# Performance work log

Hardware: AMD Instinct MI355X
Metric: run time of the kernel (lower is better)

The kernel has to match this reference:

```python
import jax, jax.numpy as jnp
import numpy as np
from jax import lax

INF = 1e4          # 'infinite' distance for chamfer transform
THETA0 = 3.0       # boundary weight decay
K_CHAMFER = 24     # exp(-24/3)~3e-4: distances beyond this are negligible
SQ2 = 1.4142135


def setup_inputs() -> dict:
    key = jax.random.key(0)
    k1, k2 = jax.random.split(key)
    inputs = jax.random.normal(k1, (32, 1, 512, 512), jnp.float32)
    targets = (jax.random.uniform(k2, (32, 1, 512, 512)) < 0.3).astype(jnp.float32)
    alpha = jnp.float32(0.25)   # config.FOCAL_ALPHA, learnable
    gamma = jnp.float32(3.0)    # config.FOCAL_GAMMA, learnable
    return {"inputs": inputs, "targets": targets, "alpha": alpha, "gamma": gamma}


def _boundary_weight(t):
    """t: (B,H,W) binary mask -> boundary-distance weight exp(-d/theta0)+0.1.
    Faithful GPU-friendly replacement for cv2 findContours/drawContours(th=3)
    + distanceTransform(L2, 3): morphological external gradient, dilated once
    (3px band), then truncated chamfer distance transform."""
    B, H, W = t.shape
    tp = jnp.pad(t, ((0, 0), (1, 1), (1, 1)))  # pad 0 so border object pixels count as edge
    eroded = lax.reduce_window(tp, jnp.inf, lax.min, (1, 3, 3), (1, 1, 1), 'VALID')
    edge = t * (1.0 - eroded)                  # contour pixels (thickness 1)
    ep = jnp.pad(edge, ((0, 0), (1, 1), (1, 1)))
    bmask = lax.reduce_window(ep, -jnp.inf, lax.max, (1, 3, 3), (1, 1, 1), 'VALID')  # thickness 3

    d = jnp.where(bmask > 0.5, 0.0, INF)
    offs = [(-1, -1, SQ2), (-1, 0, 1.0), (-1, 1, SQ2), (0, -1, 1.0),
            (0, 1, 1.0), (1, -1, SQ2), (1, 0, 1.0), (1, 1, SQ2)]

    def shift(x, di, dj):
        xp = jnp.pad(x, ((0, 0), (max(di, 0), max(-di, 0)), (max(dj, 0), max(-dj, 0))),
                     constant_values=INF)
        return xp[:, max(-di, 0):max(-di, 0) + H, max(-dj, 0):max(-dj, 0) + W]

    def step(dc, _):
        nd = dc
        for di, dj, c in offs:
            nd = jnp.minimum(nd, shift(dc, di, dj) + c)
        return nd, None

    d, _ = lax.scan(step, d, None, length=K_CHAMFER)
    return jnp.exp(-jnp.minimum(d, INF) / THETA0) + 0.1


def reference(inputs, targets, alpha, gamma):
    probs = jax.nn.sigmoid(inputs)
    smooth = 1e-6
    eps = 1e-7

    # --- dice (smp binary, from_logits, global dims=(0,2)) ---
    inter = jnp.sum(probs * targets)
    card = jnp.sum(probs) + jnp.sum(targets)
    dice_score = (2.0 * inter + smooth) / jnp.maximum(card + smooth, eps)
    dice = jnp.where(jnp.sum(targets) > 0, 1.0 - dice_score, 0.0)

    # --- adaptive focal ---
    a = jnp.clip(alpha, 0.1, 0.9)
    g = jnp.clip(gamma, 1.0, 5.0)
    st = targets * 0.95 + 0.025  # label smoothing
    bce_el = st * jax.nn.softplus(-inputs) + (1.0 - st) * jax.nn.softplus(inputs)
    p_t = st * probs + (1.0 - st) * (1.0 - probs)
    a_t = st * a + (1.0 - st) * (1.0 - a)
    focal = jnp.mean(a_t * (1.0 - p_t) ** g * bce_el)

    # --- BCEWithLogits, pos_weight=7 ---
    bce = jnp.mean(7.0 * targets * jax.nn.softplus(-inputs)
                   + (1.0 - targets) * jax.nn.softplus(inputs))

    # --- dynamic tversky, class_weight=3 ---
    pos_ratio = jnp.mean(targets)
    da = 0.7 * (1.0 + pos_ratio)
    db = 0.3 * (2.0 - pos_ratio)
    tp = inter
    fn = jnp.sum(targets * (1.0 - probs))
    fp = jnp.sum((1.0 - targets) * probs) * 3.0
    tversky = 1.0 - (tp + smooth) / (tp + da * fn + db * fp + smooth)

    # --- boundary loss (preds detached in original) ---
    t2 = targets[:, 0]
    w = _boundary_weight(t2)
    p = jnp.clip(lax.stop_gradient(probs[:, 0]), 1e-7, 1.0 - 1e-7)
    bnd_bce = -(t2 * jnp.log(p) + (1.0 - t2) * jnp.log1p(-p))
    boundary = jnp.mean(jnp.mean(bnd_bce * w, axis=(1, 2)))

    return 0.35 * dice + 0.25 * focal + 0.15 * bce + 0.15 * tversky + 0.1 * boundary
```

## Files before the change

kernel.cpp:

```cpp
#include <hip/hip_runtime.h>

typedef unsigned long long u64;
typedef unsigned int u32;

#define HH 512
#define WW 512
#define BATCH 32
#define NPIX (BATCH*HH*WW)
#define NQ (NPIX/4)
#define NWORDS (NPIX/64)
#define WPI (HH*WW/64)
#define WPR (WW/64)
#define MAIN_BLOCKS 4096
#define MAIN_THREADS 256
#define MAIN_IT 2
#define QCAP 1024
#define WINMASK ((((1ULL<<49)-1)) << 8)

__device__ __forceinline__ float hw_exp2(float x) { return __builtin_amdgcn_exp2f(x); }
__device__ __forceinline__ float hw_log2(float x) { return __builtin_amdgcn_logf(x); }

__global__ __launch_bounds__(256) void pack_kernel(const float* __restrict__ t,
                                                   u64* __restrict__ bits) {
    int stride = gridDim.x * 256;
    for (int i = blockIdx.x * 256 + threadIdx.x; i < NPIX; i += stride) {
        u64 m = __ballot(t[i] > 0.5f);
        if ((threadIdx.x & 63) == 0) bits[i >> 6] = m;
    }
}

__global__ __launch_bounds__(256) void stencil_kernel(const u64* __restrict__ tb,
                                                      u64* __restrict__ bmbits) {
    int wi = blockIdx.x * 256 + threadIdx.x;
    if (wi >= NWORDS) return;
    int img = wi >> 12;
    int loc = wi & (WPI - 1);
    int y = loc >> 3;
    int wx = loc & (WPR - 1);
    const u64* base = tb + img * WPI;

    u64 w[5][5];
    #pragma unroll
    for (int r = 0; r < 5; ++r) {
        int yy = y + r - 2;
        #pragma unroll
        for (int c = 0; c < 5; ++c) {
            int xx = wx + c - 2;
            w[r][c] = (yy >= 0 && yy < HH && xx >= 0 && xx < WPR) ? base[yy * WPR + xx] : 0ULL;
        }
    }

    u64 ha[5][3];
    #pragma unroll
    for (int r = 0; r < 5; ++r)
        #pragma unroll
        for (int j = 0; j < 3; ++j) {
            u64 C = w[r][j + 1], L = w[r][j], R = w[r][j + 2];
            ha[r][j] = ((C << 1) | (L >> 63)) & C & ((C >> 1) | (R << 63));
        }

    u64 eg[3][3];
    #pragma unroll
    for (int i = 0; i < 3; ++i)
        #pragma unroll
        for (int j = 0; j < 3; ++j) {
            u64 er = ha[i][j] & ha[i + 1][j] & ha[i + 2][j];
            eg[i][j] = w[i + 1][j + 1] & ~er;
        }

    u64 out = 0ULL;
    #pragma unroll
    for (int i = 0; i < 3; ++i) {
        u64 E = eg[i][1], L = eg[i][0], R = eg[i][2];
        out |= ((E << 1) | (L >> 63)) | E | ((E >> 1) | (R << 63));
    }
    bmbits[wi] = out;
}

__device__ __forceinline__ int rowscan(const u64* __restrict__ row, int x0) {
    int s = x0 - 32;
    int wi = s >> 6;
    int sh = s & 63;
    u64 lo = (wi >= 0 && wi < WPR) ? row[wi] : 0ULL;
    u64 hi = ((wi + 1) < WPR) ? row[wi + 1] : 0ULL;
    u64 win = sh ? ((lo >> sh) | (hi << (64 - sh))) : lo;
    win &= WINMASK;
    u64 left = win << 32;
    u64 right = win >> 32;
    int dl = left ? (__builtin_clzll(left) + 1) : 99;
    int dr = right ? __builtin_ctzll(right) : 99;
    return dl < dr ? dl : dr;
}

__device__ __forceinline__ float search_weight(const u64* __restrict__ img, int pix) {
    const float L2E = 1.44269504f;
    int x0 = pix & (WW - 1);
    int y0 = (pix >> 9) & (HH - 1);
    float best = 1e9f;
    for (int ady = 0; ady <= 24; ++ady) {
        if ((float)ady >= best) break;
        int hd = 99;
        int yU = y0 - ady;
        if (yU >= 0) hd = rowscan(img + yU * WPR, x0);
        int yD = y0 + ady;
        if (ady > 0 && yD < HH) {
            int h2 = rowscan(img + yD * WPR, x0);
            hd = h2 < hd ? h2 : hd;
        }
        if (hd <= 24) {
            float h = (float)hd, ay = (float)ady;
            float mx = fmaxf(h, ay), mn = fminf(h, ay);
            best = fminf(best, mx + 0.4142135f * mn);
        }
    }
    return (best < 1e8f) ? (hw_exp2(best * (-L2E / 3.0f)) + 0.1f) : 0.1f;
}

__global__ __launch_bounds__(MAIN_THREADS, 6) void main_kernel(
        const float4* __restrict__ x4, const u64* __restrict__ tbits,
        const u64* __restrict__ bmbits,
        const float* __restrict__ alpha_p, const float* __restrict__ gamma_p,
        double* __restrict__ partials) {
    __shared__ u64 qdata[QCAP];
    __shared__ int lcount;
    __shared__ double red[4][6];

    if (threadIdx.x == 0) lcount = 0;
    __syncthreads();

    const float a = fminf(fmaxf(alpha_p[0], 0.1f), 0.9f);
    const float one_m_a = 1.0f - a;
    const float g = fminf(fmaxf(gamma_p[0], 1.0f), 5.0f);
    const float gr = rintf(g);
    const bool gint = (g == gr);
    const int gi = (int)gr;
    const float LOGCLIP = 16.11809565f;
    const float L2E = 1.44269504f;
    const float LN2 = 0.69314718f;

    float s_p = 0.f, s_pt = 0.f, s_f = 0.f, s_b = 0.f, s_bnd_bm = 0.f, s_bnd_q = 0.f;
    int c_t = 0;

    #pragma unroll 1
    for (int it = 0; it < MAIN_IT; ++it) {
        int q = (it * MAIN_BLOCKS + blockIdx.x) * MAIN_THREADS + threadIdx.x;
        float4 xv4 = x4[q];
        int pix0 = q * 4;
        int sh = pix0 & 63;
        u64 tw = tbits[pix0 >> 6] >> sh;
        u64 bw = bmbits[pix0 >> 6] >> sh;
        float xs[4] = {xv4.x, xv4.y, xv4.z, xv4.w};

        #pragma unroll
        for (int k = 0; k < 4; ++k) {
            float xv = xs[k];
            int tb = (int)((tw >> k) & 1ULL);
            int bm = (int)((bw >> k) & 1ULL);

            float ax = fabsf(xv);
            float e  = hw_exp2(ax * -L2E);
            float rc = __builtin_amdgcn_rcpf(1.0f + e);
            float p  = (xv >= 0.0f) ? rc : e * rc;
            float l1pe = hw_log2(1.0f + e) * LN2;
            float sp_neg = fmaxf(-xv, 0.0f) + l1pe;
            float sp_pos = sp_neg + xv;

            float bce_el = sp_neg + (tb ? 0.025f : 0.975f) * xv;
            float q95 = 0.95f * p;
            float u   = tb ? (0.975f - q95) : (0.025f + q95);
            float a_t = tb ? a : one_m_a;
            float pw;
            if (gint) {
                float u2 = u * u;
                pw = (gi == 1) ? u : (gi == 2) ? u2 : (gi == 3) ? u2 * u
                   : (gi == 4) ? u2 * u2 : u2 * u2 * u;
            } else {
                pw = hw_exp2(g * hw_log2(u));
            }
            float focal_el = a_t * pw * bce_el;

            float bce2 = tb ? 7.0f * sp_neg : sp_pos;
            float bnd  = fminf(tb ? sp_neg : sp_pos, LOGCLIP);

            if (bm) {
                s_bnd_bm += bnd;
            } else {
                int slot = atomicAdd(&lcount, 1);
                if (slot < QCAP) {
                    qdata[slot] = ((u64)(u32)(pix0 + k) << 32) | (u64)__float_as_uint(bnd);
                } else {
                    s_bnd_q += bnd * search_weight(bmbits + ((pix0 + k) >> 18) * WPI, pix0 + k);
                }
            }

            s_p  += p;
            c_t  += tb;
            s_pt += tb ? p : 0.0f;
            s_f  += focal_el;
            s_b  += bce2;
        }
    }

    __syncthreads();
    int n = lcount < QCAP ? lcount : QCAP;
    for (int j = threadIdx.x; j < n; j += MAIN_THREADS) {
        u64 v = qdata[j];
        int pix = (int)(v >> 32);
        float bnd = __uint_as_float((u32)v);
        s_bnd_q += bnd * search_weight(bmbits + (pix >> 18) * WPI, pix);
    }

    double d_p = s_p, d_t = (double)c_t, d_pt = s_pt, d_f = s_f, d_b = s_b;
    double d_bnd = (double)s_bnd_bm * 1.1 + (double)s_bnd_q;

    #pragma unroll
    for (int off = 32; off > 0; off >>= 1) {
        d_p   += __shfl_down(d_p, off);
        d_t   += __shfl_down(d_t, off);
        d_pt  += __shfl_down(d_pt, off);
        d_f   += __shfl_down(d_f, off);
        d_b   += __shfl_down(d_b, off);
        d_bnd += __shfl_down(d_bnd, off);
    }

    int lane = threadIdx.x & 63, wid = threadIdx.x >> 6;
    if (lane == 0) {
        red[wid][0] = d_p;  red[wid][1] = d_t;  red[wid][2] = d_pt;
        red[wid][3] = d_f;  red[wid][4] = d_b;  red[wid][5] = d_bnd;
    }
    __syncthreads();
    if (threadIdx.x == 0) {
        #pragma unroll
        for (int i = 0; i < 6; ++i)
            partials[blockIdx.x * 6 + i] = red[0][i] + red[1][i] + red[2][i] + red[3][i];
    }
}

__global__ __launch_bounds__(256) void reduce_kernel(const double* __restrict__ partials,
                                                     float* __restrict__ out) {
    double s[6] = {0, 0, 0, 0, 0, 0};
    for (int b = threadIdx.x; b < MAIN_BLOCKS; b += 256)
        #pragma unroll
        for (int i = 0; i < 6; ++i) s[i] += partials[b * 6 + i];

    #pragma unroll
    for (int off = 32; off > 0; off >>= 1)
        #pragma unroll
        for (int i = 0; i < 6; ++i) s[i] += __shfl_down(s[i], off);

    __shared__ double red[4][6];
    int lane = threadIdx.x & 63, wid = threadIdx.x >> 6;
    if (lane == 0)
        #pragma unroll
        for (int i = 0; i < 6; ++i) red[wid][i] = s[i];
    __syncthreads();

    if (threadIdx.x == 0) {
        double S_p = red[0][0] + red[1][0] + red[2][0] + red[3][0];
        double S_t = red[0][1] + red[1][1] + red[2][1] + red[3][1];
        double S_pt = red[0][2] + red[1][2] + red[2][2] + red[3][2];
        double S_f = red[0][3] + red[1][3] + red[2][3] + red[3][3];
        double S_b = red[0][4] + red[1][4] + red[2][4] + red[3][4];
        double S_bnd = red[0][5] + red[1][5] + red[2][5] + red[3][5];
        const double N = (double)NPIX;
        double inter = S_pt;
        double card = S_p + S_t;
        double dice_score = (2.0 * inter + 1e-6) / fmax(card + 1e-6, 1e-7);
        double dice = (S_t > 0.0) ? (1.0 - dice_score) : 0.0;
        double focal = S_f / N;
        double bce = S_b / N;
        double pos_ratio = S_t / N;
        double da = 0.7 * (1.0 + pos_ratio);
        double db = 0.3 * (2.0 - pos_ratio);
        double fn = S_t - S_pt;
        double fp = (S_p - S_pt) * 3.0;
        double tversky = 1.0 - (S_pt + 1e-6) / (S_pt + da * fn + db * fp + 1e-6);
        double bnd = S_bnd / N;
        out[0] = (float)(0.35 * dice + 0.25 * focal + 0.15 * bce + 0.15 * tversky + 0.1 * bnd);
    }
}

extern "C" void kernel_launch(void* const* d_in, const int* in_sizes, int n_in,
                              void* d_out, int out_size, void* d_ws, size_t ws_size,
                              hipStream_t stream) {
    const float* inputs  = (const float*)d_in[0];
    const float* targets = (const float*)d_in[1];
    const float* alpha_p = (const float*)d_in[2];
    const float* gamma_p = (const float*)d_in[3];
    float* out = (float*)d_out;

    char* ws = (char*)d_ws;
    double* partials = (double*)ws;
    u64* tbits  = (u64*)(ws + 262144);
    u64* bmbits = (u64*)(ws + 262144 + NWORDS * 8);

    pack_kernel<<<4096, 256, 0, stream>>>(targets, tbits);
    stencil_kernel<<<NWORDS / 256, 256, 0, stream>>>(tbits, bmbits);
    main_kernel<<<MAIN_BLOCKS, MAIN_THREADS, 0, stream>>>(
        (const float4*)inputs, tbits, bmbits, alpha_p, gamma_p, partials);
    reduce_kernel<<<1, 256, 0, stream>>>(partials, out);
}
```

Measured before the change: 49.98 us.

## Fuse pack and stencil, compact off-band pixels into global queue, last-block reduce

Packing the targets to bits and computing the boundary band now happen in one kernel. It stages each 32-row strip in shared memory and emits a global list of off-band pixel indices. A separate search kernel then runs the distance search over that compacted list, which removes the per-block shared queue and the divergent in-loop search from the main kernel. The main kernel processes four float4s per thread, and the last-arriving block does the final reduction, which drops the reduce launch but adds a memset, global atomics and a buffer sized to the number of off-band pixels.

```diff
diff --git a/kernel.cpp b/kernel.cpp
--- a/kernel.cpp
+++ b/kernel.cpp
@@ -7,56 +7,79 @@
 #define WW 512
 #define BATCH 32
 #define NPIX (BATCH*HH*WW)
-#define NQ (NPIX/4)
-#define NWORDS (NPIX/64)
 #define WPI (HH*WW/64)
 #define WPR (WW/64)
-#define MAIN_BLOCKS 4096
+
+#define STRIPS 16
+#define PS_BLOCKS (BATCH*STRIPS)
+
+#define MAIN_BLOCKS 2048
 #define MAIN_THREADS 256
-#define MAIN_IT 2
-#define QCAP 1024
+
+#define SEARCH_BLOCKS 512
 #define WINMASK ((((1ULL<<49)-1)) << 8)
+
+#define WS_CTR    0
+#define WS_MAINP  4096
+#define WS_SRCHP  102400
+#define WS_TBITS  131072
+#define WS_BMBITS 1179648
+#define WS_QBUF   2228224
 
 __device__ __forceinline__ float hw_exp2(float x) { return __builtin_amdgcn_exp2f(x); }
 __device__ __forceinline__ float hw_log2(float x) { return __builtin_amdgcn_logf(x); }
 
-__global__ __launch_bounds__(256) void pack_kernel(const float* __restrict__ t,
-                                                   u64* __restrict__ bits) {
-    int stride = gridDim.x * 256;
-    for (int i = blockIdx.x * 256 + threadIdx.x; i < NPIX; i += stride) {
-        u64 m = __ballot(t[i] > 0.5f);
-        if ((threadIdx.x & 63) == 0) bits[i >> 6] = m;
-    }
-}
-
-__global__ __launch_bounds__(256) void stencil_kernel(const u64* __restrict__ tb,
-                                                      u64* __restrict__ bmbits) {
-    int wi = blockIdx.x * 256 + threadIdx.x;
-    if (wi >= NWORDS) return;
-    int img = wi >> 12;
-    int loc = wi & (WPI - 1);
-    int y = loc >> 3;
-    int wx = loc & (WPR - 1);
-    const u64* base = tb + img * WPI;
+__global__ __launch_bounds__(256) void pack_stencil_kernel(
+        const float4* __restrict__ t4, u64* __restrict__ tbits,
+        u64* __restrict__ bmbits, u32* __restrict__ qcnt, u32* __restrict__ qbuf) {
+    __shared__ u64 lw[36][9];
+    __shared__ int blkcnt;
+    __shared__ u32 gbase;
+
+    const int blk = blockIdx.x;
+    const int img = blk >> 4;
+    const int strip = blk & 15;
+    const int row0 = strip * 32;
+    if (threadIdx.x == 0) blkcnt = 0;
+
+    unsigned char* lb = (unsigned char*)lw;
+    #pragma unroll
+    for (int it = 0; it < 9; ++it) {
+        int i = it * 256 + threadIdx.x;
+        int r = i >> 6, c = i & 63;
+        int gy = row0 - 2 + r;
+        unsigned b = 0;
+        if (gy >= 0 && gy < HH) {
+            int base = img * (HH*WW/4) + gy * (WW/4) + c * 2;
+            float4 lo = t4[base], hi = t4[base + 1];
+            b =  (lo.x > 0.5f)       | ((lo.y > 0.5f) << 1)
+              | ((lo.z > 0.5f) << 2) | ((lo.w > 0.5f) << 3)
+              | ((hi.x > 0.5f) << 4) | ((hi.y > 0.5f) << 5)
+              | ((hi.z > 0.5f) << 6) | ((hi.w > 0.5f) << 7);
+        }
+        lb[r * 72 + c] = (unsigned char)b;
+    }
+    __syncthreads();
+
+    const int r  = threadIdx.x >> 3;
+    const int wc = threadIdx.x & 7;
 
     u64 w[5][5];
     #pragma unroll
-    for (int r = 0; r < 5; ++r) {
-        int yy = y + r - 2;
-        #pragma unroll
-        for (int c = 0; c < 5; ++c) {
-            int xx = wx + c - 2;
-            w[r][c] = (yy >= 0 && yy < HH && xx >= 0 && xx < WPR) ? base[yy * WPR + xx] : 0ULL;
-        }
-    }
+    for (int dr = 0; dr < 5; ++dr)
+        #pragma unroll
+        for (int dc = 0; dc < 5; ++dc) {
+            int cc = wc + dc - 2;
+            w[dr][dc] = (cc >= 0 && cc < 8) ? lw[r + dr][cc] : 0ULL;
+        }
 
     u64 ha[5][3];
     #pragma unroll
-    for (int r = 0; r < 5; ++r)
+    for (int rr = 0; rr < 5; ++rr)
         #pragma unroll
         for (int j = 0; j < 3; ++j) {
-            u64 C = w[r][j + 1], L = w[r][j], R = w[r][j + 2];
-            ha[r][j] = ((C << 1) | (L >> 63)) & C & ((C >> 1) | (R << 63));
+            u64 C = w[rr][j + 1], L = w[rr][j], R = w[rr][j + 2];
+            ha[rr][j] = ((C << 1) | (L >> 63)) & C & ((C >> 1) | (R << 63));
         }
 
     u64 eg[3][3];
@@ -74,7 +97,24 @@
         u64 E = eg[i][1], L = eg[i][0], R = eg[i][2];
         out |= ((E << 1) | (L >> 63)) | E | ((E >> 1) | (R << 63));
     }
-    bmbits[wi] = out;
+
+    int gw = img * WPI + (row0 + r) * WPR + wc;
+    tbits[gw]  = w[2][2];
+    bmbits[gw] = out;
+
+    u64 m = ~out;
+    int nz = __popcll(m);
+    int lbase = atomicAdd(&blkcnt, nz);
+    __syncthreads();
+    if (threadIdx.x == 0) gbase = atomicAdd(qcnt, (u32)blkcnt);
+    __syncthreads();
+    u32 o = gbase + (u32)lbase;
+    int pixbase = img * (HH * WW) + (row0 + r) * WW + wc * 64;
+    while (m) {
+        int b = __builtin_ctzll(m);
+        qbuf[o++] = (u32)(pixbase + b);
+        m &= m - 1;
+    }
 }
 
 __device__ __forceinline__ int rowscan(const u64* __restrict__ row, int x0) {
@@ -116,17 +156,45 @@
     return (best < 1e8f) ? (hw_exp2(best * (-L2E / 3.0f)) + 0.1f) : 0.1f;
 }
 
-__global__ __launch_bounds__(MAIN_THREADS, 6) void main_kernel(
+__global__ __launch_bounds__(256) void search_kernel(
+        const float* __restrict__ x, const u64* __restrict__ tbits,
+        const u64* __restrict__ bmbits, const u32* __restrict__ qcnt,
+        const u32* __restrict__ qbuf, double* __restrict__ searchP) {
+    const float L2E = 1.44269504f, LN2 = 0.69314718f, LOGCLIP = 16.11809565f;
+    int n = (int)*qcnt;
+    float acc = 0.f;
+    for (int i = blockIdx.x * 256 + threadIdx.x; i < n; i += SEARCH_BLOCKS * 256) {
+        int pix = (int)qbuf[i];
+        float xv = x[pix];
+        int tb = (int)((tbits[pix >> 6] >> (pix & 63)) & 1ULL);
+        float ax = fabsf(xv);
+        float e = hw_exp2(ax * -L2E);
+        float l1pe = hw_log2(1.0f + e) * LN2;
+        float sp_neg = fmaxf(-xv, 0.0f) + l1pe;
+        float sp = tb ? sp_neg : (sp_neg + xv);
+        float bnd = fminf(sp, LOGCLIP);
+        float wgt = search_weight(bmbits + (pix >> 18) * WPI, pix);
+        acc += bnd * wgt;
+    }
+    double d = acc;
+    #pragma unroll
+    for (int off = 32; off > 0; off >>= 1) d += __shfl_down(d, off);
+    __shared__ double red[4];
+    int lane = threadIdx.x & 63, wid = threadIdx.x >> 6;
+    if (lane == 0) red[wid] = d;
+    __syncthreads();
+    if (threadIdx.x == 0)
+        searchP[blockIdx.x] = red[0] + red[1] + red[2] + red[3];
+}
+
+__global__ __launch_bounds__(256) void main_kernel(
         const float4* __restrict__ x4, const u64* __restrict__ tbits,
         const u64* __restrict__ bmbits,
         const float* __restrict__ alpha_p, const float* __restrict__ gamma_p,
-        double* __restrict__ partials) {
-    __shared__ u64 qdata[QCAP];
-    __shared__ int lcount;
+        double* __restrict__ mainP, const double* __restrict__ searchP,
+        u32* __restrict__ cnt, float* __restrict__ out) {
     __shared__ double red[4][6];
-
-    if (threadIdx.x == 0) lcount = 0;
-    __syncthreads();
+    __shared__ int amLast;
 
     const float a = fminf(fmaxf(alpha_p[0], 0.1f), 0.9f);
     const float one_m_a = 1.0f - a;
@@ -138,34 +206,39 @@
     const float L2E = 1.44269504f;
     const float LN2 = 0.69314718f;
 
-    float s_p = 0.f, s_pt = 0.f, s_f = 0.f, s_b = 0.f, s_bnd_bm = 0.f, s_bnd_q = 0.f;
+    float s_p = 0.f, s_pt = 0.f, s_f = 0.f, s_b = 0.f, s_bnd = 0.f;
     int c_t = 0;
 
-    #pragma unroll 1
-    for (int it = 0; it < MAIN_IT; ++it) {
-        int q = (it * MAIN_BLOCKS + blockIdx.x) * MAIN_THREADS + threadIdx.x;
-        float4 xv4 = x4[q];
-        int pix0 = q * 4;
-        int sh = pix0 & 63;
-        u64 tw = tbits[pix0 >> 6] >> sh;
-        u64 bw = bmbits[pix0 >> 6] >> sh;
-        float xs[4] = {xv4.x, xv4.y, xv4.z, xv4.w};
-
+    const int base = blockIdx.x * 1024 + threadIdx.x;
+    float4 xv[4];
+    u32 tn[4], bn[4];
+    #pragma unroll
+    for (int j = 0; j < 4; ++j) {
+        int q = base + j * 256;
+        xv[j] = x4[q];
+        int sh = (q & 15) * 4;
+        tn[j] = (u32)((tbits[q >> 4]  >> sh) & 0xfULL);
+        bn[j] = (u32)((bmbits[q >> 4] >> sh) & 0xfULL);
+    }
+
+    #pragma unroll
+    for (int j = 0; j < 4; ++j) {
+        float xs[4] = {xv[j].x, xv[j].y, xv[j].z, xv[j].w};
         #pragma unroll
         for (int k = 0; k < 4; ++k) {
-            float xv = xs[k];
-            int tb = (int)((tw >> k) & 1ULL);
-            int bm = (int)((bw >> k) & 1ULL);
-
-            float ax = fabsf(xv);
+            float xvv = xs[k];
+            int tb = (int)((tn[j] >> k) & 1u);
+            int bm = (int)((bn[j] >> k) & 1u);
+
+            float ax = fabsf(xvv);
             float e  = hw_exp2(ax * -L2E);
             float rc = __builtin_amdgcn_rcpf(1.0f + e);
-            float p  = (xv >= 0.0f) ? rc : e * rc;
+            float p  = (xvv >= 0.0f) ? rc : e * rc;
             float l1pe = hw_log2(1.0f + e) * LN2;
-            float sp_neg = fmaxf(-xv, 0.0f) + l1pe;
-            float sp_pos = sp_neg + xv;
-
-            float bce_el = sp_neg + (tb ? 0.025f : 0.975f) * xv;
+            float sp_neg = fmaxf(-xvv, 0.0f) + l1pe;
+            float sp_pos = sp_neg + xvv;
+
+            float bce_el = sp_neg + (tb ? 0.025f : 0.975f) * xvv;
             float q95 = 0.95f * p;
             float u   = tb ? (0.975f - q95) : (0.025f + q95);
             float a_t = tb ? a : one_m_a;
@@ -182,36 +255,17 @@
             float bce2 = tb ? 7.0f * sp_neg : sp_pos;
             float bnd  = fminf(tb ? sp_neg : sp_pos, LOGCLIP);
 
-            if (bm) {
-                s_bnd_bm += bnd;
-            } else {
-                int slot = atomicAdd(&lcount, 1);
-                if (slot < QCAP) {
-                    qdata[slot] = ((u64)(u32)(pix0 + k) << 32) | (u64)__float_as_uint(bnd);
-                } else {
-                    s_bnd_q += bnd * search_weight(bmbits + ((pix0 + k) >> 18) * WPI, pix0 + k);
-                }
-            }
-
-            s_p  += p;
-            c_t  += tb;
-            s_pt += tb ? p : 0.0f;
-            s_f  += focal_el;
-            s_b  += bce2;
-        }
-    }
-
-    __syncthreads();
-    int n = lcount < QCAP ? lcount : QCAP;
-    for (int j = threadIdx.x; j < n; j += MAIN_THREADS) {
-        u64 v = qdata[j];
-        int pix = (int)(v >> 32);
-        float bnd = __uint_as_float((u32)v);
-        s_bnd_q += bnd * search_weight(bmbits + (pix >> 18) * WPI, pix);
+            s_p   += p;
+            c_t   += tb;
+            s_pt  += tb ? p : 0.0f;
+            s_f   += focal_el;
+            s_b   += bce2;
+            s_bnd += bm ? bnd : 0.0f;
+        }
     }
 
     double d_p = s_p, d_t = (double)c_t, d_pt = s_pt, d_f = s_f, d_b = s_b;
-    double d_bnd = (double)s_bnd_bm * 1.1 + (double)s_bnd_q;
+    double d_bnd = (double)s_bnd * 1.1;
 
     #pragma unroll
     for (int off = 32; off > 0; off >>= 1) {
@@ -232,51 +286,57 @@
     if (threadIdx.x == 0) {
         #pragma unroll
         for (int i = 0; i < 6; ++i)
-            partials[blockIdx.x * 6 + i] = red[0][i] + red[1][i] + red[2][i] + red[3][i];
-    }
-}
-
-__global__ __launch_bounds__(256) void reduce_kernel(const double* __restrict__ partials,
-                                                     float* __restrict__ out) {
-    double s[6] = {0, 0, 0, 0, 0, 0};
-    for (int b = threadIdx.x; b < MAIN_BLOCKS; b += 256)
-        #pragma unroll
-        for (int i = 0; i < 6; ++i) s[i] += partials[b * 6 + i];
-
-    #pragma unroll
-    for (int off = 32; off > 0; off >>= 1)
-        #pragma unroll
-        for (int i = 0; i < 6; ++i) s[i] += __shfl_down(s[i], off);
-
-    __shared__ double red[4][6];
-    int lane = threadIdx.x & 63, wid = threadIdx.x >> 6;
-    if (lane == 0)
-        #pragma unroll
-        for (int i = 0; i < 6; ++i) red[wid][i] = s[i];
-    __syncthreads();
-
-    if (threadIdx.x == 0) {
-        double S_p = red[0][0] + red[1][0] + red[2][0] + red[3][0];
-        double S_t = red[0][1] + red[1][1] + red[2][1] + red[3][1];
-        double S_pt = red[0][2] + red[1][2] + red[2][2] + red[3][2];
-        double S_f = red[0][3] + red[1][3] + red[2][3] + red[3][3];
-        double S_b = red[0][4] + red[1][4] + red[2][4] + red[3][4];
-        double S_bnd = red[0][5] + red[1][5] + red[2][5] + red[3][5];
-        const double N = (double)NPIX;
-        double inter = S_pt;
-        double card = S_p + S_t;
-        double dice_score = (2.0 * inter + 1e-6) / fmax(card + 1e-6, 1e-7);
-        double dice = (S_t > 0.0) ? (1.0 - dice_score) : 0.0;
-        double focal = S_f / N;
-        double bce = S_b / N;
-        double pos_ratio = S_t / N;
-        double da = 0.7 * (1.0 + pos_ratio);
-        double db = 0.3 * (2.0 - pos_ratio);
-        double fn = S_t - S_pt;
-        double fp = (S_p - S_pt) * 3.0;
-        double tversky = 1.0 - (S_pt + 1e-6) / (S_pt + da * fn + db * fp + 1e-6);
-        double bnd = S_bnd / N;
-        out[0] = (float)(0.35 * dice + 0.25 * focal + 0.15 * bce + 0.15 * tversky + 0.1 * bnd);
+            mainP[i * MAIN_BLOCKS + blockIdx.x] =
+                red[0][i] + red[1][i] + red[2][i] + red[3][i];
+        __threadfence();
+        u32 old = atomicAdd(cnt, 1u);
+        amLast = (old == MAIN_BLOCKS - 1);
+    }
+    __syncthreads();
+
+    if (amLast) {
+        __threadfence();
+        double s[6] = {0, 0, 0, 0, 0, 0};
+        for (int b = threadIdx.x; b < MAIN_BLOCKS; b += 256)
+            #pragma unroll
+            for (int i = 0; i < 6; ++i) s[i] += mainP[i * MAIN_BLOCKS + b];
+        for (int b = threadIdx.x; b < SEARCH_BLOCKS; b += 256)
+            s[5] += searchP[b];
+
+        #pragma unroll
+        for (int off = 32; off > 0; off >>= 1)
+            #pragma unroll
+            for (int i = 0; i < 6; ++i) s[i] += __shfl_down(s[i], off);
+
+        __syncthreads();
+        if (lane == 0)
+            #pragma unroll
+            for (int i = 0; i < 6; ++i) red[wid][i] = s[i];
+        __syncthreads();
+
+        if (threadIdx.x == 0) {
+            double S_p = red[0][0] + red[1][0] + red[2][0] + red[3][0];
+            double S_t = red[0][1] + red[1][1] + red[2][1] + red[3][1];
+            double S_pt = red[0][2] + red[1][2] + red[2][2] + red[3][2];
+            double S_f = red[0][3] + red[1][3] + red[2][3] + red[3][3];
+            double S_b = red[0][4] + red[1][4] + red[2][4] + red[3][4];
+            double S_bnd = red[0][5] + red[1][5] + red[2][5] + red[3][5];
+            const double N = (double)NPIX;
+            double inter = S_pt;
+            double card = S_p + S_t;
+            double dice_score = (2.0 * inter + 1e-6) / fmax(card + 1e-6, 1e-7);
+            double dice = (S_t > 0.0) ? (1.0 - dice_score) : 0.0;
+            double focal = S_f / N;
+            double bce = S_b / N;
+            double pos_ratio = S_t / N;
+            double da = 0.7 * (1.0 + pos_ratio);
+            double db = 0.3 * (2.0 - pos_ratio);
+            double fn = S_t - S_pt;
+            double fp = (S_p - S_pt) * 3.0;
+            double tversky = 1.0 - (S_pt + 1e-6) / (S_pt + da * fn + db * fp + 1e-6);
+            double bnd = S_bnd / N;
+            out[0] = (float)(0.35 * dice + 0.25 * focal + 0.15 * bce + 0.15 * tversky + 0.1 * bnd);
+        }
     }
 }
 
@@ -290,13 +350,22 @@
     float* out = (float*)d_out;
 
     char* ws = (char*)d_ws;
-    double* partials = (double*)ws;
-    u64* tbits  = (u64*)(ws + 262144);
-    u64* bmbits = (u64*)(ws + 262144 + NWORDS * 8);
-
-    pack_kernel<<<4096, 256, 0, stream>>>(targets, tbits);
-    stencil_kernel<<<NWORDS / 256, 256, 0, stream>>>(tbits, bmbits);
-    main_kernel<<<MAIN_BLOCKS, MAIN_THREADS, 0, stream>>>(
-        (const float4*)inputs, tbits, bmbits, alpha_p, gamma_p, partials);
-    reduce_kernel<<<1, 256, 0, stream>>>(partials, out);
-}
+    u32*    ctrs    = (u32*)(ws + WS_CTR);
+    double* mainP   = (double*)(ws + WS_MAINP);
+    double* searchP = (double*)(ws + WS_SRCHP);
+    u64*    tbits   = (u64*)(ws + WS_TBITS);
+    u64*    bmbits  = (u64*)(ws + WS_BMBITS);
+    u32*    qbuf    = (u32*)(ws + WS_QBUF);
+
+    hipMemsetAsync(ctrs, 0, 8, stream);
+
+    pack_stencil_kernel<<<PS_BLOCKS, 256, 0, stream>>>(
+        (const float4*)targets, tbits, bmbits, &ctrs[0], qbuf);
+
+    search_kernel<<<SEARCH_BLOCKS, 256, 0, stream>>>(
+        inputs, tbits, bmbits, &ctrs[0], qbuf, searchP);
+
+    main_kernel<<<MAIN_BLOCKS, 256, 0, stream>>>(
+        (const float4*)inputs, tbits, bmbits, alpha_p, gamma_p,
+        mainP, searchP, &ctrs[1], out);
+}
```

After: 95.73 us. 91.5% more time.
